# Kernel optimization log

Measured on AMD Instinct MI355X. Metric: run time of the kernel, lower is better.

The kernel has to match this reference:

```python
import jax, jax.numpy as jnp
import numpy as np
from functools import partial

V, H, B, T, L = 32000, 1024, 64, 64, 4
EOS = 2


def setup_inputs() -> dict:
    key = jax.random.key(0)
    ks = jax.random.split(key, 10)
    s = 1.0 / np.sqrt(H)
    return {
        "max_len": T,
        "tgt": jax.random.randint(ks[0], (B, T), 0, V),
        "h0": jax.random.normal(ks[1], (L, B, H), jnp.float32),
        "c0": jax.random.normal(ks[2], (L, B, H), jnp.float32),
        "embedding": jax.random.normal(ks[3], (V, H), jnp.float32) * s,
        "W_ih": jax.random.normal(ks[4], (L, 4 * H, H), jnp.float32) * s,
        "W_hh": jax.random.normal(ks[5], (L, 4 * H, H), jnp.float32) * s,
        "b_ih": jax.random.normal(ks[6], (L, 4 * H), jnp.float32) * s,
        "b_hh": jax.random.normal(ks[7], (L, 4 * H), jnp.float32) * s,
        "W_cls": jax.random.normal(ks[8], (V, H), jnp.float32) * s,
        "b_cls": jax.random.normal(ks[9], (V,), jnp.float32) * s,
    }


def _lstm_cell(x, h, c, Wi, Wh, bi, bh):
    # gates: [B, 4H] in torch order (i, f, g, o)
    g = x @ Wi.T + bi + h @ Wh.T + bh
    i, f, gg, o = jnp.split(g, 4, axis=-1)
    c2 = jax.nn.sigmoid(f) * c + jax.nn.sigmoid(i) * jnp.tanh(gg)
    h2 = jax.nn.sigmoid(o) * jnp.tanh(c2)
    return h2, c2


def reference(max_len, tgt, h0, c0, embedding, W_ih, W_hh, b_ih, b_hh, W_cls, b_cls):
    # step i>0 uses embedding of tgt[:, i-1].
    batch = tgt.shape[0]
    x0 = jnp.broadcast_to(embedding[EOS], (batch, embedding.shape[1]))
    tf_in = embedding[tgt[:, : max_len - 1]]              # [B, T-1, H]
    inputs = jnp.concatenate([x0[:, None, :], tf_in], axis=1)  # [B, T, H]
    inputs = jnp.swapaxes(inputs, 0, 1)                   # [T, B, H]

    def step(carry, x):
        h, c = carry  # each [L, B, H]
        hs, cs = [], []
        inp = x
        for l in range(L):  # 4 stacked LSTM cells, h of cell l feeds cell l+1
            hn, cn = _lstm_cell(inp, h[l], c[l], W_ih[l], W_hh[l], b_ih[l], b_hh[l])
            hs.append(hn)
            cs.append(cn)
            inp = hn
        h = jnp.stack(hs)
        c = jnp.stack(cs)
        logp = jax.nn.log_softmax(h[L - 1] @ W_cls.T + b_cls, axis=-1)  # [B, V]
        return (h, c), logp

    (h, c), out = jax.lax.scan(step, (h0, c0), inputs)
    return out, h, c  # out: [T, B, V]
```

## Files before the change

kernel.cpp:

```cpp
#include <hip/hip_runtime.h>

using u16 = unsigned short;
using u32 = unsigned int;

typedef __bf16 bf16x8 __attribute__((ext_vector_type(8)));
typedef float  f32x4  __attribute__((ext_vector_type(4)));
typedef u16    u16x8  __attribute__((ext_vector_type(8)));

static constexpr int kV = 32000, kH = 1024, kB = 64, kT = 64, kL = 4, kEOS = 2;

struct Flag { int v; int pad[15]; };

__device__ __forceinline__ u16 f2bf(float f) {
  u32 u = __float_as_uint(f);
  u = (u + 0x7fffu + ((u >> 16) & 1u)) >> 16;
  return (u16)u;
}
__device__ __forceinline__ float sigf(float x)   { return 1.0f / (1.0f + __expf(-x)); }
__device__ __forceinline__ float tanhf_(float x) { return 1.0f - 2.0f / (__expf(2.0f * x) + 1.0f); }

typedef const __attribute__((address_space(1))) u32* gas_ptr;
typedef __attribute__((address_space(3))) u32*       las_ptr;
__device__ __forceinline__ void async16(const u16* g, u16* l) {
  __builtin_amdgcn_global_load_lds((gas_ptr)g, (las_ptr)l, 16, 0, 0);
}

__device__ __forceinline__ void spin_ge(const int* p, int tgt) {
  while (__hip_atomic_load(p, __ATOMIC_RELAXED, __HIP_MEMORY_SCOPE_AGENT) < tgt)
    __builtin_amdgcn_s_sleep(2);
}

__device__ __forceinline__ size_t packed_off(int b, int k) {
  return (size_t)(((b >> 4) * 32 + (k >> 5)) * 512 + (((k >> 3) & 3) * 16 + (b & 15)) * 8 + (k & 7));
}


__global__ void pack_lstm(const float* __restrict__ Wih, const float* __restrict__ Whh,
                          u16* __restrict__ wpack) {
  const int cid  = blockIdx.x * 256 + threadIdx.x;
  const int lane = cid & 63;
  const int cf   = (cid >> 6) & 3;
  const int kk   = (cid >> 8) & 31;
  const int mt   = (cid >> 13) & 1;
  const int blk  = cid >> 14;
  const int lay = blk >> 6, cb = blk & 63;
  const int wr = cf * 1024 + cb * 16 + (lane & 15);
  const int kb = kk * 32 + (lane >> 4) * 8;
  const float* src = (mt ? Whh : Wih) + ((size_t)lay * 4096 + wr) * 1024 + kb;
  const float4* s4 = (const float4*)src;
  float4 v0 = s4[0], v1 = s4[1];
  u16x8 r;
  r[0]=f2bf(v0.x); r[1]=f2bf(v0.y); r[2]=f2bf(v0.z); r[3]=f2bf(v0.w);
  r[4]=f2bf(v1.x); r[5]=f2bf(v1.y); r[6]=f2bf(v1.z); r[7]=f2bf(v1.w);
  *(u16x8*)(wpack + (size_t)cid * 8) = r;
}

__global__ void pack_cls(const float* __restrict__ W, u16* __restrict__ o) {
  const size_t cid = (size_t)blockIdx.x * 256 + threadIdx.x;
  const float4* s4 = (const float4*)(W + cid * 8);
  float4 v0 = s4[0], v1 = s4[1];
  u16x8 r;
  r[0]=f2bf(v0.x); r[1]=f2bf(v0.y); r[2]=f2bf(v0.z); r[3]=f2bf(v0.w);
  r[4]=f2bf(v1.x); r[5]=f2bf(v1.y); r[6]=f2bf(v1.z); r[7]=f2bf(v1.w);
  *(u16x8*)(o + cid * 8) = r;
}

__global__ void pack_x(const float* __restrict__ emb, const int* __restrict__ tgt,
                       u16* __restrict__ X) {
  const int cid = blockIdx.x * 256 + threadIdx.x;
  const int kc = cid & 127, b = (cid >> 7) & 63, t = cid >> 13;
  const int tok = (t == 0) ? kEOS : tgt[b * 64 + t - 1];
  const float4* s4 = (const float4*)(emb + (size_t)tok * 1024 + kc * 8);
  float4 v0 = s4[0], v1 = s4[1];
  u16x8 r;
  r[0]=f2bf(v0.x); r[1]=f2bf(v0.y); r[2]=f2bf(v0.z); r[3]=f2bf(v0.w);
  r[4]=f2bf(v1.x); r[5]=f2bf(v1.y); r[6]=f2bf(v1.z); r[7]=f2bf(v1.w);
  *(u16x8*)(X + (size_t)t * 65536 + packed_off(b, kc * 8)) = r;
}

__global__ void pack_init(const float* __restrict__ h0, const float* __restrict__ bih,
                          const float* __restrict__ bhh, u16* __restrict__ hball,
                          float* __restrict__ bsum) {
  const int cid = blockIdx.x * 256 + threadIdx.x;
  if (cid < 32768) {
    const int kc = cid & 127, row = cid >> 7;
    const int lay = row >> 6, b = row & 63;
    const float4* s4 = (const float4*)(h0 + (size_t)cid * 8);
    float4 v0 = s4[0], v1 = s4[1];
    u16x8 r;
    r[0]=f2bf(v0.x); r[1]=f2bf(v0.y); r[2]=f2bf(v0.z); r[3]=f2bf(v0.w);
    r[4]=f2bf(v1.x); r[5]=f2bf(v1.y); r[6]=f2bf(v1.z); r[7]=f2bf(v1.w);
    *(u16x8*)(hball + (size_t)lay * 65 * 65536 + packed_off(b, kc * 8)) = r;
  } else {
    const int i = cid - 32768;
    bsum[i] = bih[i] + bhh[i];
  }
}

__global__ void __launch_bounds__(512)
lstm_coop(const u16* __restrict__ wpack, const u16* __restrict__ xall,
          u16* __restrict__ hball, const float* __restrict__ bsum,
          const float* __restrict__ c0, float* __restrict__ outh, float* __restrict__ outc,
          Flag* flags) {
  __shared__ u16 stg[3][32][512];
  __shared__ float Gc[2][64][68];

  const int tid = threadIdx.x, lane = tid & 63, wave = tid >> 6;
  const int l15 = lane & 15, l4 = lane >> 4;
  const int cmat = wave >> 2, cwc = (wave >> 1) & 1, ckh = wave & 1;
  const int blk = blockIdx.x, lay = blk >> 6, cb = blk & 63, u0 = cb << 4;
  const int ub = tid >> 3, uu = (tid & 7) * 2;

  float creg0 = c0[((size_t)lay * 64 + ub) * 1024 + u0 + uu];
  float creg1 = c0[((size_t)lay * 64 + ub) * 1024 + u0 + uu + 1];
  float bsv[8];
  #pragma unroll
  for (int g = 0; g < 4; ++g) {
    bsv[g]     = bsum[lay * 4096 + g * 1024 + u0 + uu];
    bsv[4 + g] = bsum[lay * 4096 + g * 1024 + u0 + uu + 1];
  }

  const size_t wbase = (size_t)blk * 131072;
  bf16x8 breg[2][16];
  #pragma unroll
  for (int ci = 0; ci < 2; ++ci)
    #pragma unroll
    for (int j = 0; j < 16; ++j)
      breg[ci][j] = *(const bf16x8*)(wpack + wbase
          + (size_t)(((cmat * 32 + 2 * j + ckh) * 4) + cwc * 2 + ci) * 512 + lane * 8);

  u16* hlay = hball + (size_t)lay * 65 * 65536;
  const u16* hprev = (lay == 0) ? xall : (hball + (size_t)(lay - 1) * 65 * 65536);

  #pragma unroll 1
  for (int t = 0; t < kT; ++t) {
    if (t > 0 && tid < 64)               spin_ge(&flags[lay * 64 + tid].v, t);
    if (lay > 0 && tid >= 64 && tid < 128) spin_ge(&flags[(lay - 1) * 64 + (tid - 64)].v, t + 1);
    __syncthreads();

    const u16* xsrc = (lay == 0) ? (xall + (size_t)t * 65536)
                                 : (hprev + (size_t)(t + 1) * 65536);
    const u16* hsrc = hlay + (size_t)t * 65536;

    auto STAGE = [&](int c) {
      #pragma unroll
      for (int q = 0; q < 4; ++q) {
        const int j = wave * 4 + q;
        const int m2 = j >> 4, mt = (j >> 2) & 3, ksl = j & 3;
        const u16* g = (m2 ? hsrc : xsrc) + (size_t)((mt * 32 + c * 4 + ksl) * 512) + lane * 8;
        async16(g, &stg[c % 3][m2 * 16 + mt * 4 + ksl][0]);
      }
    };

    f32x4 acc[4][2] = {};
    STAGE(0); STAGE(1);
    #pragma unroll
    for (int c = 0; c < 8; ++c) {
      if (c < 7) asm volatile("s_waitcnt vmcnt(4)" ::: "memory");
      else       asm volatile("s_waitcnt vmcnt(0)" ::: "memory");
      __builtin_amdgcn_s_barrier();
      asm volatile("" ::: "memory");
      if (c < 6) STAGE(c + 2);
      const u16* As = &stg[c % 3][cmat * 16][0];
      #pragma unroll
      for (int s = 0; s < 2; ++s) {
        const int ksl = 2 * s + ckh;
        bf16x8 a[4];
        #pragma unroll
        for (int m = 0; m < 4; ++m)
          a[m] = *(const bf16x8*)(As + (m * 4 + ksl) * 512 + lane * 8);
        #pragma unroll
        for (int m = 0; m < 4; ++m) {
          acc[m][0] = __builtin_amdgcn_mfma_f32_16x16x32_bf16(a[m], breg[0][2 * c + s], acc[m][0], 0, 0, 0);
          acc[m][1] = __builtin_amdgcn_mfma_f32_16x16x32_bf16(a[m], breg[1][2 * c + s], acc[m][1], 0, 0, 0);
        }
      }
    }

    if (ckh == 0) {
      #pragma unroll
      for (int m = 0; m < 4; ++m)
        #pragma unroll
        for (int ci = 0; ci < 2; ++ci)
          #pragma unroll
          for (int r = 0; r < 4; ++r)
            Gc[cmat][m * 16 + l4 * 4 + r][cwc * 32 + ci * 16 + l15] = acc[m][ci][r];
    }
    __syncthreads();
    if (ckh == 1) {
      #pragma unroll
      for (int m = 0; m < 4; ++m)
        #pragma unroll
        for (int ci = 0; ci < 2; ++ci)
          #pragma unroll
          for (int r = 0; r < 4; ++r)
            Gc[cmat][m * 16 + l4 * 4 + r][cwc * 32 + ci * 16 + l15] += acc[m][ci][r];
    }
    __syncthreads();

    float2 sg[4];
    #pragma unroll
    for (int g = 0; g < 4; ++g) {
      const int col = g * 16 + uu;
      const float2 v0 = *(const float2*)&Gc[0][ub][col];
      const float2 v1 = *(const float2*)&Gc[1][ub][col];
      sg[g] = make_float2(v0.x + v1.x, v0.y + v1.y);
    }
    u16 hv[2];
    #pragma unroll
    for (int p = 0; p < 2; ++p) {
      const float gi = (p ? sg[0].y : sg[0].x) + bsv[p * 4 + 0];
      const float gf = (p ? sg[1].y : sg[1].x) + bsv[p * 4 + 1];
      const float gg = (p ? sg[2].y : sg[2].x) + bsv[p * 4 + 2];
      const float go = (p ? sg[3].y : sg[3].x) + bsv[p * 4 + 3];
      const float cr = (p == 0) ? creg0 : creg1;
      const float c2 = sigf(gf) * cr + sigf(gi) * tanhf_(gg);
      const float h2 = sigf(go) * tanhf_(c2);
      if (p == 0) creg0 = c2; else creg1 = c2;
      hv[p] = f2bf(h2);
      if (t == kT - 1) {
        outh[((size_t)lay * 64 + ub) * 1024 + u0 + uu + p] = h2;
        outc[((size_t)lay * 64 + ub) * 1024 + u0 + uu + p] = c2;
      }
    }
    const u32 hpair = (u32)hv[0] | ((u32)hv[1] << 16);
    u32* hdst = (u32*)(hlay + (size_t)(t + 1) * 65536 + packed_off(ub, u0 + uu));
    __hip_atomic_store(hdst, hpair, __ATOMIC_RELAXED, __HIP_MEMORY_SCOPE_AGENT);

    __syncthreads();
    if (tid == 0)
      __hip_atomic_store(&flags[lay * 64 + cb].v, t + 1, __ATOMIC_RELAXED, __HIP_MEMORY_SCOPE_AGENT);
  }
}

__global__ void __launch_bounds__(256)
cls_gemm(const u16* __restrict__ A, const u16* __restrict__ Bw,
         const float* __restrict__ bcls, float* __restrict__ out) {
  __shared__ u16 sA[2][4096], sB[2][4096];
  const int tid = threadIdx.x, lane = tid & 63, wave = tid >> 6;
  const int wm = wave >> 1, wc = wave & 1;
  const int l15 = lane & 15, l4 = lane >> 4;
  const int bn = blockIdx.x, bm = blockIdx.y;
  const u16* Ab = A  + (size_t)bm * 131072;
  const u16* Bb = Bw + (size_t)bn * 131072;

  auto STAGE = [&](int kk) {
    u16* dA = sA[kk & 1]; u16* dB = sB[kk & 1];
    #pragma unroll
    for (int q = 0; q < 4; ++q) {
      const int u = wave * 4 + q;
      if (u < 8) {
        const u16* g = Ab + (size_t)(u >> 2) * 65536 + (size_t)(((u & 3) * 32 + kk) * 512) + lane * 8;
        async16(g, dA + u * 512);
      } else {
        const int v = u & 7;
        const u16* g = Bb + (size_t)((v & 1) * 64 + lane) * 1024 + kk * 32 + (v >> 1) * 8;
        async16(g, dB + v * 512);
      }
    }
  };

  f32x4 acc[4][4] = {};
  STAGE(0);
  for (int kk = 0; kk < 32; ++kk) {
    if (kk < 31) { STAGE(kk + 1); asm volatile("s_waitcnt vmcnt(4)" ::: "memory"); }
    else         asm volatile("s_waitcnt vmcnt(0)" ::: "memory");
    __builtin_amdgcn_s_barrier();
    asm volatile("" ::: "memory");
    const u16* aS = sA[kk & 1]; const u16* bS = sB[kk & 1];
    bf16x8 av[4], bv[4];
    #pragma unroll
    for (int mi = 0; mi < 4; ++mi) av[mi] = *(const bf16x8*)(aS + (wm * 4 + mi) * 512 + lane * 8);
    #pragma unroll
    for (int ci = 0; ci < 4; ++ci) bv[ci] = *(const bf16x8*)(bS + l4 * 1024 + (wc * 64 + ci * 16 + l15) * 8);
    #pragma unroll
    for (int mi = 0; mi < 4; ++mi)
      #pragma unroll
      for (int ci = 0; ci < 4; ++ci)
        acc[mi][ci] = __builtin_amdgcn_mfma_f32_16x16x32_bf16(av[mi], bv[ci], acc[mi][ci], 0, 0, 0);
    asm volatile("" ::: "memory");
    __builtin_amdgcn_s_barrier();
  }
  #pragma unroll
  for (int ci = 0; ci < 4; ++ci) {
    const int col = bn * 128 + wc * 64 + ci * 16 + l15;
    const float bc = bcls[col];
    #pragma unroll
    for (int mi = 0; mi < 4; ++mi) {
      #pragma unroll
      for (int r = 0; r < 4; ++r) {
        const int row = bm * 128 + wm * 64 + mi * 16 + l4 * 4 + r;
        out[(size_t)row * 32000 + col] = acc[mi][ci][r] + bc;
      }
    }
  }
}

__global__ void __launch_bounds__(256)
cls_gemm_f32(const u16* __restrict__ A, const float* __restrict__ Bw,
             const float* __restrict__ bcls, float* __restrict__ out) {
  __shared__ u16 sA[2][4096], sB[2][4096];
  const int tid = threadIdx.x, lane = tid & 63, wave = tid >> 6;
  const int wm = wave >> 1, wc = wave & 1;
  const int l15 = lane & 15, l4 = lane >> 4;
  const int bn = blockIdx.x, bm = blockIdx.y;
  const u16*  Ab = A  + (size_t)bm * 131072;
  const float* Bb = Bw + (size_t)bn * 131072;

  auto LOADB = [&](int kk, u16x8* rb) {
    #pragma unroll
    for (int q = 0; q < 2; ++q) {
      const int p = tid + q * 256, row = p & 127, khi = p >> 7;
      const float4* s4 = (const float4*)(Bb + (size_t)row * 1024 + kk * 32 + khi * 8);
      float4 v0 = s4[0], v1 = s4[1];
      u16x8 r;
      r[0]=f2bf(v0.x); r[1]=f2bf(v0.y); r[2]=f2bf(v0.z); r[3]=f2bf(v0.w);
      r[4]=f2bf(v1.x); r[5]=f2bf(v1.y); r[6]=f2bf(v1.z); r[7]=f2bf(v1.w);
      rb[q] = r;
    }
  };
  auto WRITEB = [&](int kk, const u16x8* rb) {
    u16* dB = sB[kk & 1];
    #pragma unroll
    for (int q = 0; q < 2; ++q) {
      const int p = tid + q * 256;
      *(u16x8*)(dB + p * 8) = rb[q];
    }
  };
  auto STAGE_A = [&](int kk) {
    u16* dA = sA[kk & 1];
    #pragma unroll
    for (int q = 0; q < 2; ++q) {
      const int v = wave * 2 + q;
      const u16* g = Ab + (size_t)(v >> 2) * 65536 + (size_t)(((v & 3) * 32 + kk) * 512) + lane * 8;
      async16(g, dA + v * 512);
    }
  };

  f32x4 acc[4][4] = {};
  {
    u16x8 rb[2];
    LOADB(0, rb); STAGE_A(0); WRITEB(0, rb);
  }
  for (int kk = 0; kk < 32; ++kk) {
    if (kk < 31) {
      u16x8 rb[2];
      LOADB(kk + 1, rb);
      STAGE_A(kk + 1);
      WRITEB(kk + 1, rb);
    } else {
      asm volatile("s_waitcnt vmcnt(0)" ::: "memory");
    }
    __builtin_amdgcn_s_barrier();
    asm volatile("" ::: "memory");
    const u16* aS = sA[kk & 1]; const u16* bS = sB[kk & 1];
    bf16x8 av[4], bv[4];
    #pragma unroll
    for (int mi = 0; mi < 4; ++mi) av[mi] = *(const bf16x8*)(aS + (wm * 4 + mi) * 512 + lane * 8);
    #pragma unroll
    for (int ci = 0; ci < 4; ++ci) bv[ci] = *(const bf16x8*)(bS + l4 * 1024 + (wc * 64 + ci * 16 + l15) * 8);
    #pragma unroll
    for (int mi = 0; mi < 4; ++mi)
      #pragma unroll
      for (int ci = 0; ci < 4; ++ci)
        acc[mi][ci] = __builtin_amdgcn_mfma_f32_16x16x32_bf16(av[mi], bv[ci], acc[mi][ci], 0, 0, 0);
    asm volatile("" ::: "memory");
    __builtin_amdgcn_s_barrier();
  }
  #pragma unroll
  for (int ci = 0; ci < 4; ++ci) {
    const int col = bn * 128 + wc * 64 + ci * 16 + l15;
    const float bc = bcls[col];
    #pragma unroll
    for (int mi = 0; mi < 4; ++mi) {
      #pragma unroll
      for (int r = 0; r < 4; ++r) {
        const int row = bm * 128 + wm * 64 + mi * 16 + l4 * 4 + r;
        out[(size_t)row * 32000 + col] = acc[mi][ci][r] + bc;
      }
    }
  }
}

__global__ void __launch_bounds__(256)
lsm_k(float* __restrict__ out) {
  __shared__ float red[256];
  const int r = blockIdx.x;
  float* p = out + (size_t)r * 32000;
  const float4* p4 = (const float4*)p;
  float m = -3.0e38f;
  for (int v = threadIdx.x; v < 8000; v += 256) {
    const float4 x = p4[v];
    m = fmaxf(m, fmaxf(fmaxf(x.x, x.y), fmaxf(x.z, x.w)));
  }
  red[threadIdx.x] = m; __syncthreads();
  for (int s2 = 128; s2 > 0; s2 >>= 1) {
    if ((int)threadIdx.x < s2) red[threadIdx.x] = fmaxf(red[threadIdx.x], red[threadIdx.x + s2]);
    __syncthreads();
  }
  m = red[0]; __syncthreads();
  float s = 0.0f;
  for (int v = threadIdx.x; v < 8000; v += 256) {
    const float4 x = p4[v];
    s += __expf(x.x - m) + __expf(x.y - m) + __expf(x.z - m) + __expf(x.w - m);
  }
  red[threadIdx.x] = s; __syncthreads();
  for (int s2 = 128; s2 > 0; s2 >>= 1) {
    if ((int)threadIdx.x < s2) red[threadIdx.x] += red[threadIdx.x + s2];
    __syncthreads();
  }
  const float z = m + logf(red[0]);
  float4* q4 = (float4*)p;
  for (int v = threadIdx.x; v < 8000; v += 256) {
    float4 x = p4[v];
    x.x -= z; x.y -= z; x.z -= z; x.w -= z;
    q4[v] = x;
  }
}

extern "C" void kernel_launch(void* const* d_in, const int* in_sizes, int n_in,
                              void* d_out, int out_size, void* d_ws, size_t ws_size,
                              hipStream_t stream) {
  (void)in_sizes; (void)n_in; (void)out_size;
  const int*   tgt  = (const int*)d_in[1];
  const float* h0   = (const float*)d_in[2];
  const float* c0   = (const float*)d_in[3];
  const float* emb  = (const float*)d_in[4];
  const float* Wih  = (const float*)d_in[5];
  const float* Whh  = (const float*)d_in[6];
  const float* bih  = (const float*)d_in[7];
  const float* bhh  = (const float*)d_in[8];
  const float* Wcls = (const float*)d_in[9];
  const float* bcls = (const float*)d_in[10];

  float* out  = (float*)d_out;
  float* outh = out + (size_t)kT * kB * kV;
  float* outc = outh + (size_t)kL * kB * kH;

  const size_t SZ_WPACK = 67108864;
  const size_t SZ_WCLS  = 65536000;
  const size_t SZ_X     = 8388608;
  const size_t SZ_HBALL = 34078720;
  const size_t SZ_BSUM  = 65536;
  const size_t SZ_FLAGS = 16384;
  const size_t FULL_REQ = SZ_WPACK + SZ_WCLS + SZ_X + SZ_HBALL + SZ_BSUM + SZ_FLAGS;
  const bool full = (ws_size >= FULL_REQ);

  char* ws = (char*)d_ws;
  size_t off = 0;
  u16* wpack = (u16*)(ws + off); off += SZ_WPACK;
  u16* wclsb = nullptr;
  if (full) { wclsb = (u16*)(ws + off); off += SZ_WCLS; }
  u16*   X     = (u16*)(ws + off); off += SZ_X;
  u16*   hball = (u16*)(ws + off); off += SZ_HBALL;
  float* bsum  = (float*)(ws + off); off += SZ_BSUM;
  Flag*  flags = (Flag*)(ws + off);  off += SZ_FLAGS;

  pack_lstm<<<16384, 256, 0, stream>>>(Wih, Whh, wpack);
  if (full) pack_cls<<<16000, 256, 0, stream>>>(Wcls, wclsb);
  pack_x   <<<2048,  256, 0, stream>>>(emb, tgt, X);
  pack_init<<<192,   256, 0, stream>>>(h0, bih, bhh, hball, bsum);
  hipMemsetAsync(flags, 0, SZ_FLAGS, stream);

  void* args[] = { (void*)&wpack, (void*)&X, (void*)&hball, (void*)&bsum,
                   (void*)&c0, (void*)&outh, (void*)&outc, (void*)&flags };
  hipLaunchCooperativeKernel((const void*)lstm_coop, dim3(256), dim3(512), args, 0, stream);

  const u16* h3a = hball + (size_t)3 * 65 * 65536 + 65536;
  if (full) cls_gemm    <<<dim3(250, 32), 256, 0, stream>>>(h3a, wclsb, bcls, out);
  else      cls_gemm_f32<<<dim3(250, 32), 256, 0, stream>>>(h3a, Wcls,  bcls, out);
  lsm_k<<<4096, 256, 0, stream>>>(out);
}
```

Measured before the change: 1.451 ms.

## Fuse log-softmax partial reductions into classifier GEMM and widen LSTM blocks

The classifier GEMM epilogue now computes per-tile row max and sum-exp partials. A small reduction kernel combines them into log-normalizers, and a final pass subtracts them, replacing the three-pass log-softmax that re-read the logits twice. Separately, the cooperative LSTM kernel moves to 1024 threads per block with 16 waves that each own one column tile, double- rather than triple-buffered staging, and a single four-way LDS reduction of gate partials. This cuts register pressure per wave and one barrier per step, but adds per-row syncthreads in the GEMM epilogue and a shallower load pipeline.

```diff
diff --git a/kernel.cpp b/kernel.cpp
--- a/kernel.cpp
+++ b/kernel.cpp
@@ -97,44 +97,42 @@
   }
 }
 
-__global__ void __launch_bounds__(512)
+__global__ void __launch_bounds__(1024, 4)
 lstm_coop(const u16* __restrict__ wpack, const u16* __restrict__ xall,
           u16* __restrict__ hball, const float* __restrict__ bsum,
           const float* __restrict__ c0, float* __restrict__ outh, float* __restrict__ outc,
           Flag* flags) {
-  __shared__ u16 stg[3][32][512];
-  __shared__ float Gc[2][64][68];
+  __shared__ u16 stg[2][32][512];
+  __shared__ float Gc[4][64][66];
 
   const int tid = threadIdx.x, lane = tid & 63, wave = tid >> 6;
   const int l15 = lane & 15, l4 = lane >> 4;
-  const int cmat = wave >> 2, cwc = (wave >> 1) & 1, ckh = wave & 1;
+  const int cmat = wave >> 3, cwc = (wave >> 1) & 3, ckh = wave & 1;
   const int blk = blockIdx.x, lay = blk >> 6, cb = blk & 63, u0 = cb << 4;
-  const int ub = tid >> 3, uu = (tid & 7) * 2;
-
-  float creg0 = c0[((size_t)lay * 64 + ub) * 1024 + u0 + uu];
-  float creg1 = c0[((size_t)lay * 64 + ub) * 1024 + u0 + uu + 1];
-  float bsv[8];
-  #pragma unroll
-  for (int g = 0; g < 4; ++g) {
-    bsv[g]     = bsum[lay * 4096 + g * 1024 + u0 + uu];
-    bsv[4 + g] = bsum[lay * 4096 + g * 1024 + u0 + uu + 1];
-  }
+  const int ub = tid >> 4, uu = tid & 15;
+
+  float creg = c0[((size_t)lay * 64 + ub) * 1024 + u0 + uu];
+  float bsv[4];
+  #pragma unroll
+  for (int g = 0; g < 4; ++g) bsv[g] = bsum[lay * 4096 + g * 1024 + u0 + uu];
 
   const size_t wbase = (size_t)blk * 131072;
-  bf16x8 breg[2][16];
-  #pragma unroll
-  for (int ci = 0; ci < 2; ++ci)
-    #pragma unroll
-    for (int j = 0; j < 16; ++j)
-      breg[ci][j] = *(const bf16x8*)(wpack + wbase
-          + (size_t)(((cmat * 32 + 2 * j + ckh) * 4) + cwc * 2 + ci) * 512 + lane * 8);
+  bf16x8 breg[16];
+  #pragma unroll
+  for (int j = 0; j < 16; ++j)
+    breg[j] = *(const bf16x8*)(wpack + wbase
+        + (size_t)(((cmat * 32 + 2 * j + ckh) * 4) + cwc) * 512 + lane * 8);
+
+  const int j0 = wave * 2, j1 = wave * 2 + 1;
+  const int m2a = j0 >> 4, mta = (j0 >> 2) & 3, ksla = j0 & 3;
+  const int m2b = j1 >> 4, mtb = (j1 >> 2) & 3, kslb = j1 & 3;
 
   u16* hlay = hball + (size_t)lay * 65 * 65536;
   const u16* hprev = (lay == 0) ? xall : (hball + (size_t)(lay - 1) * 65 * 65536);
 
   #pragma unroll 1
   for (int t = 0; t < kT; ++t) {
-    if (t > 0 && tid < 64)               spin_ge(&flags[lay * 64 + tid].v, t);
+    if (t > 0 && tid < 64)                 spin_ge(&flags[lay * 64 + tid].v, t);
     if (lay > 0 && tid >= 64 && tid < 128) spin_ge(&flags[(lay - 1) * 64 + (tid - 64)].v, t + 1);
     __syncthreads();
 
@@ -142,26 +140,25 @@
                                  : (hprev + (size_t)(t + 1) * 65536);
     const u16* hsrc = hlay + (size_t)t * 65536;
 
+    const u16* ga = (m2a ? hsrc : xsrc) + (size_t)((mta * 32 + ksla) * 512) + lane * 8;
+    const u16* gb = (m2b ? hsrc : xsrc) + (size_t)((mtb * 32 + kslb) * 512) + lane * 8;
+    u16* da = &stg[0][m2a * 16 + mta * 4 + ksla][0];
+    u16* db = &stg[0][m2b * 16 + mtb * 4 + kslb][0];
+
     auto STAGE = [&](int c) {
-      #pragma unroll
-      for (int q = 0; q < 4; ++q) {
-        const int j = wave * 4 + q;
-        const int m2 = j >> 4, mt = (j >> 2) & 3, ksl = j & 3;
-        const u16* g = (m2 ? hsrc : xsrc) + (size_t)((mt * 32 + c * 4 + ksl) * 512) + lane * 8;
-        async16(g, &stg[c % 3][m2 * 16 + mt * 4 + ksl][0]);
-      }
+      async16(ga + (size_t)c * 2048, da + (c & 1) * 16384);
+      async16(gb + (size_t)c * 2048, db + (c & 1) * 16384);
     };
 
-    f32x4 acc[4][2] = {};
-    STAGE(0); STAGE(1);
+    f32x4 acc[4] = {};
+    STAGE(0);
     #pragma unroll
     for (int c = 0; c < 8; ++c) {
-      if (c < 7) asm volatile("s_waitcnt vmcnt(4)" ::: "memory");
-      else       asm volatile("s_waitcnt vmcnt(0)" ::: "memory");
+      asm volatile("s_waitcnt vmcnt(0)" ::: "memory");
       __builtin_amdgcn_s_barrier();
       asm volatile("" ::: "memory");
-      if (c < 6) STAGE(c + 2);
-      const u16* As = &stg[c % 3][cmat * 16][0];
+      if (c < 7) STAGE(c + 1);
+      const u16* As = &stg[c & 1][cmat * 16][0];
       #pragma unroll
       for (int s = 0; s < 2; ++s) {
         const int ksl = 2 * s + ckh;
@@ -170,72 +167,83 @@
         for (int m = 0; m < 4; ++m)
           a[m] = *(const bf16x8*)(As + (m * 4 + ksl) * 512 + lane * 8);
         #pragma unroll
-        for (int m = 0; m < 4; ++m) {
-          acc[m][0] = __builtin_amdgcn_mfma_f32_16x16x32_bf16(a[m], breg[0][2 * c + s], acc[m][0], 0, 0, 0);
-          acc[m][1] = __builtin_amdgcn_mfma_f32_16x16x32_bf16(a[m], breg[1][2 * c + s], acc[m][1], 0, 0, 0);
-        }
+        for (int m = 0; m < 4; ++m)
+          acc[m] = __builtin_amdgcn_mfma_f32_16x16x32_bf16(a[m], breg[2 * c + s], acc[m], 0, 0, 0);
       }
     }
 
-    if (ckh == 0) {
+    {
+      const int q = cmat * 2 + ckh;
       #pragma unroll
       for (int m = 0; m < 4; ++m)
         #pragma unroll
-        for (int ci = 0; ci < 2; ++ci)
-          #pragma unroll
-          for (int r = 0; r < 4; ++r)
-            Gc[cmat][m * 16 + l4 * 4 + r][cwc * 32 + ci * 16 + l15] = acc[m][ci][r];
+        for (int r = 0; r < 4; ++r)
+          Gc[q][m * 16 + l4 * 4 + r][cwc * 16 + l15] = acc[m][r];
     }
     __syncthreads();
-    if (ckh == 1) {
-      #pragma unroll
-      for (int m = 0; m < 4; ++m)
-        #pragma unroll
-        for (int ci = 0; ci < 2; ++ci)
-          #pragma unroll
-          for (int r = 0; r < 4; ++r)
-            Gc[cmat][m * 16 + l4 * 4 + r][cwc * 32 + ci * 16 + l15] += acc[m][ci][r];
-    }
-    __syncthreads();
-
-    float2 sg[4];
+
+    float sg[4];
     #pragma unroll
     for (int g = 0; g < 4; ++g) {
       const int col = g * 16 + uu;
-      const float2 v0 = *(const float2*)&Gc[0][ub][col];
-      const float2 v1 = *(const float2*)&Gc[1][ub][col];
-      sg[g] = make_float2(v0.x + v1.x, v0.y + v1.y);
-    }
-    u16 hv[2];
-    #pragma unroll
-    for (int p = 0; p < 2; ++p) {
-      const float gi = (p ? sg[0].y : sg[0].x) + bsv[p * 4 + 0];
-      const float gf = (p ? sg[1].y : sg[1].x) + bsv[p * 4 + 1];
-      const float gg = (p ? sg[2].y : sg[2].x) + bsv[p * 4 + 2];
-      const float go = (p ? sg[3].y : sg[3].x) + bsv[p * 4 + 3];
-      const float cr = (p == 0) ? creg0 : creg1;
-      const float c2 = sigf(gf) * cr + sigf(gi) * tanhf_(gg);
-      const float h2 = sigf(go) * tanhf_(c2);
-      if (p == 0) creg0 = c2; else creg1 = c2;
-      hv[p] = f2bf(h2);
-      if (t == kT - 1) {
-        outh[((size_t)lay * 64 + ub) * 1024 + u0 + uu + p] = h2;
-        outc[((size_t)lay * 64 + ub) * 1024 + u0 + uu + p] = c2;
-      }
-    }
-    const u32 hpair = (u32)hv[0] | ((u32)hv[1] << 16);
-    u32* hdst = (u32*)(hlay + (size_t)(t + 1) * 65536 + packed_off(ub, u0 + uu));
-    __hip_atomic_store(hdst, hpair, __ATOMIC_RELAXED, __HIP_MEMORY_SCOPE_AGENT);
-
+      sg[g] = Gc[0][ub][col] + Gc[1][ub][col] + Gc[2][ub][col] + Gc[3][ub][col] + bsv[g];
+    }
+    const float c2 = sigf(sg[1]) * creg + sigf(sg[0]) * tanhf_(sg[2]);
+    const float h2 = sigf(sg[3]) * tanhf_(c2);
+    creg = c2;
+    const u16 hv = f2bf(h2);
+    if (t == kT - 1) {
+      outh[((size_t)lay * 64 + ub) * 1024 + u0 + uu] = h2;
+      outc[((size_t)lay * 64 + ub) * 1024 + u0 + uu] = c2;
+    }
+    const u32 other = __shfl_xor((u32)hv, 1);
+    if ((tid & 1) == 0) {
+      const u32 hpair = (u32)hv | (other << 16);
+      u32* hdst = (u32*)(hlay + (size_t)(t + 1) * 65536 + packed_off(ub, u0 + uu));
+      __hip_atomic_store(hdst, hpair, __ATOMIC_RELAXED, __HIP_MEMORY_SCOPE_AGENT);
+    }
     __syncthreads();
     if (tid == 0)
       __hip_atomic_store(&flags[lay * 64 + cb].v, t + 1, __ATOMIC_RELAXED, __HIP_MEMORY_SCOPE_AGENT);
   }
 }
 
+#define CLS_EPILOGUE()                                                                     \
+  {                                                                                        \
+    float* sR = (float*)&sA[0][0];                                                         \
+    _Pragma("unroll")                                                                      \
+    for (int mi = 0; mi < 4; ++mi) {                                                       \
+      _Pragma("unroll")                                                                    \
+      for (int r = 0; r < 4; ++r) {                                                        \
+        float v[4];                                                                        \
+        _Pragma("unroll")                                                                  \
+        for (int ci = 0; ci < 4; ++ci) v[ci] = acc[mi][ci][r] + bc[ci];                     \
+        float mx = fmaxf(fmaxf(v[0], v[1]), fmaxf(v[2], v[3]));                            \
+        mx = fmaxf(mx, __shfl_xor(mx, 1)); mx = fmaxf(mx, __shfl_xor(mx, 2));              \
+        mx = fmaxf(mx, __shfl_xor(mx, 4)); mx = fmaxf(mx, __shfl_xor(mx, 8));              \
+        float ss = __expf(v[0]-mx) + __expf(v[1]-mx) + __expf(v[2]-mx) + __expf(v[3]-mx);  \
+        ss += __shfl_xor(ss, 1); ss += __shfl_xor(ss, 2);                                  \
+        ss += __shfl_xor(ss, 4); ss += __shfl_xor(ss, 8);                                  \
+        const int lr = wm * 64 + mi * 16 + l4 * 4 + r;                                     \
+        if (wc == 0 && l15 == 0) { sR[lr * 2] = mx; sR[lr * 2 + 1] = ss; }                 \
+        __syncthreads();                                                                   \
+        if (wc == 1 && l15 == 0) {                                                         \
+          const float m0 = sR[lr * 2], s0 = sR[lr * 2 + 1];                                \
+          const float M = fmaxf(m0, mx);                                                   \
+          const float S = s0 * __expf(m0 - M) + ss * __expf(mx - M);                       \
+          const int grow = bm * 128 + lr;                                                  \
+          pmax[(size_t)grow * 256 + bn] = M;                                               \
+          psum[(size_t)grow * 256 + bn] = S;                                               \
+        }                                                                                  \
+        __syncthreads();                                                                   \
+      }                                                                                    \
+    }                                                                                      \
+  }
+
 __global__ void __launch_bounds__(256)
 cls_gemm(const u16* __restrict__ A, const u16* __restrict__ Bw,
-         const float* __restrict__ bcls, float* __restrict__ out) {
+         const float* __restrict__ bcls, float* __restrict__ out,
+         float* __restrict__ pmax, float* __restrict__ psum) {
   __shared__ u16 sA[2][4096], sB[2][4096];
   const int tid = threadIdx.x, lane = tid & 63, wave = tid >> 6;
   const int wm = wave >> 1, wc = wave & 1;
@@ -281,24 +289,28 @@
     asm volatile("" ::: "memory");
     __builtin_amdgcn_s_barrier();
   }
+  float bc[4];
+  #pragma unroll
+  for (int ci = 0; ci < 4; ++ci) bc[ci] = bcls[bn * 128 + wc * 64 + ci * 16 + l15];
   #pragma unroll
   for (int ci = 0; ci < 4; ++ci) {
     const int col = bn * 128 + wc * 64 + ci * 16 + l15;
-    const float bc = bcls[col];
-    #pragma unroll
-    for (int mi = 0; mi < 4; ++mi) {
+    #pragma unroll
+    for (int mi = 0; mi < 4; ++mi)
       #pragma unroll
       for (int r = 0; r < 4; ++r) {
         const int row = bm * 128 + wm * 64 + mi * 16 + l4 * 4 + r;
-        out[(size_t)row * 32000 + col] = acc[mi][ci][r] + bc;
+        out[(size_t)row * 32000 + col] = acc[mi][ci][r] + bc[ci];
       }
-    }
-  }
+  }
+  __syncthreads();
+  CLS_EPILOGUE()
 }
 
 __global__ void __launch_bounds__(256)
 cls_gemm_f32(const u16* __restrict__ A, const float* __restrict__ Bw,
-             const float* __restrict__ bcls, float* __restrict__ out) {
+             const float* __restrict__ bcls, float* __restrict__ out,
+             float* __restrict__ pmax, float* __restrict__ psum) {
   __shared__ u16 sA[2][4096], sB[2][4096];
   const int tid = threadIdx.x, lane = tid & 63, wave = tid >> 6;
   const int wm = wave >> 1, wc = wave & 1;
@@ -322,10 +334,7 @@
   auto WRITEB = [&](int kk, const u16x8* rb) {
     u16* dB = sB[kk & 1];
     #pragma unroll
-    for (int q = 0; q < 2; ++q) {
-      const int p = tid + q * 256;
-      *(u16x8*)(dB + p * 8) = rb[q];
-    }
+    for (int q = 0; q < 2; ++q) *(u16x8*)(dB + (tid + q * 256) * 8) = rb[q];
   };
   auto STAGE_A = [&](int kk) {
     u16* dA = sA[kk & 1];
@@ -367,54 +376,53 @@
     asm volatile("" ::: "memory");
     __builtin_amdgcn_s_barrier();
   }
+  float bc[4];
+  #pragma unroll
+  for (int ci = 0; ci < 4; ++ci) bc[ci] = bcls[bn * 128 + wc * 64 + ci * 16 + l15];
   #pragma unroll
   for (int ci = 0; ci < 4; ++ci) {
     const int col = bn * 128 + wc * 64 + ci * 16 + l15;
-    const float bc = bcls[col];
-    #pragma unroll
-    for (int mi = 0; mi < 4; ++mi) {
+    #pragma unroll
+    for (int mi = 0; mi < 4; ++mi)
       #pragma unroll
       for (int r = 0; r < 4; ++r) {
         const int row = bm * 128 + wm * 64 + mi * 16 + l4 * 4 + r;
-        out[(size_t)row * 32000 + col] = acc[mi][ci][r] + bc;
+        out[(size_t)row * 32000 + col] = acc[mi][ci][r] + bc[ci];
       }
-    }
-  }
+  }
+  __syncthreads();
+  CLS_EPILOGUE()
 }
 
 __global__ void __launch_bounds__(256)
-lsm_k(float* __restrict__ out) {
-  __shared__ float red[256];
+lsm_red(const float* __restrict__ pmax, const float* __restrict__ psum,
+        float* __restrict__ logz) {
+  __shared__ float rm[256], rs[256];
+  const int r = blockIdx.x, b = threadIdx.x;
+  float m = -3.0e38f, s = 0.0f;
+  if (b < 250) { m = pmax[(size_t)r * 256 + b]; s = psum[(size_t)r * 256 + b]; }
+  rm[b] = m; rs[b] = s; __syncthreads();
+  for (int st = 128; st > 0; st >>= 1) {
+    if (b < st) {
+      const float m2 = rm[b + st], s2 = rs[b + st];
+      const float M = fmaxf(rm[b], m2);
+      rs[b] = rs[b] * __expf(rm[b] - M) + s2 * __expf(m2 - M);
+      rm[b] = M;
+    }
+    __syncthreads();
+  }
+  if (b == 0) logz[r] = rm[0] + logf(rs[0]);
+}
+
+__global__ void __launch_bounds__(256)
+sub_k(float* __restrict__ out, const float* __restrict__ logz) {
   const int r = blockIdx.x;
-  float* p = out + (size_t)r * 32000;
-  const float4* p4 = (const float4*)p;
-  float m = -3.0e38f;
+  const float z = logz[r];
+  float4* p = (float4*)(out + (size_t)r * 32000);
   for (int v = threadIdx.x; v < 8000; v += 256) {
-    const float4 x = p4[v];
-    m = fmaxf(m, fmaxf(fmaxf(x.x, x.y), fmaxf(x.z, x.w)));
-  }
-  red[threadIdx.x] = m; __syncthreads();
-  for (int s2 = 128; s2 > 0; s2 >>= 1) {
-    if ((int)threadIdx.x < s2) red[threadIdx.x] = fmaxf(red[threadIdx.x], red[threadIdx.x + s2]);
-    __syncthreads();
-  }
-  m = red[0]; __syncthreads();
-  float s = 0.0f;
-  for (int v = threadIdx.x; v < 8000; v += 256) {
-    const float4 x = p4[v];
-    s += __expf(x.x - m) + __expf(x.y - m) + __expf(x.z - m) + __expf(x.w - m);
-  }
-  red[threadIdx.x] = s; __syncthreads();
-  for (int s2 = 128; s2 > 0; s2 >>= 1) {
-    if ((int)threadIdx.x < s2) red[threadIdx.x] += red[threadIdx.x + s2];
-    __syncthreads();
-  }
-  const float z = m + logf(red[0]);
-  float4* q4 = (float4*)p;
-  for (int v = threadIdx.x; v < 8000; v += 256) {
-    float4 x = p4[v];
+    float4 x = p[v];
     x.x -= z; x.y -= z; x.z -= z; x.w -= z;
-    q4[v] = x;
+    p[v] = x;
   }
 }
 
@@ -443,7 +451,8 @@
   const size_t SZ_HBALL = 34078720;
   const size_t SZ_BSUM  = 65536;
   const size_t SZ_FLAGS = 16384;
-  const size_t FULL_REQ = SZ_WPACK + SZ_WCLS + SZ_X + SZ_HBALL + SZ_BSUM + SZ_FLAGS;
+  const size_t SZ_PM    = 4194304;
+  const size_t FULL_REQ = SZ_WPACK + SZ_WCLS + SZ_X + SZ_HBALL + SZ_BSUM + SZ_FLAGS + 2 * SZ_PM + 16384;
   const bool full = (ws_size >= FULL_REQ);
 
   char* ws = (char*)d_ws;
@@ -455,6 +464,9 @@
   u16*   hball = (u16*)(ws + off); off += SZ_HBALL;
   float* bsum  = (float*)(ws + off); off += SZ_BSUM;
   Flag*  flags = (Flag*)(ws + off);  off += SZ_FLAGS;
+  float* pmax  = (float*)(ws + off); off += SZ_PM;
+  float* psum  = (float*)(ws + off); off += SZ_PM;
+  float* logz  = (float*)(ws + off); off += 16384;
 
   pack_lstm<<<16384, 256, 0, stream>>>(Wih, Whh, wpack);
   if (full) pack_cls<<<16000, 256, 0, stream>>>(Wcls, wclsb);
@@ -464,10 +476,11 @@
 
   void* args[] = { (void*)&wpack, (void*)&X, (void*)&hball, (void*)&bsum,
                    (void*)&c0, (void*)&outh, (void*)&outc, (void*)&flags };
-  hipLaunchCooperativeKernel((const void*)lstm_coop, dim3(256), dim3(512), args, 0, stream);
+  hipLaunchCooperativeKernel((const void*)lstm_coop, dim3(256), dim3(1024), args, 0, stream);
 
   const u16* h3a = hball + (size_t)3 * 65 * 65536 + 65536;
-  if (full) cls_gemm    <<<dim3(250, 32), 256, 0, stream>>>(h3a, wclsb, bcls, out);
-  else      cls_gemm_f32<<<dim3(250, 32), 256, 0, stream>>>(h3a, Wcls,  bcls, out);
-  lsm_k<<<4096, 256, 0, stream>>>(out);
-}
+  if (full) cls_gemm    <<<dim3(250, 32), 256, 0, stream>>>(h3a, wclsb, bcls, out, pmax, psum);
+  else      cls_gemm_f32<<<dim3(250, 32), 256, 0, stream>>>(h3a, Wcls,  bcls, out, pmax, psum);
+  lsm_red<<<4096, 256, 0, stream>>>(pmax, psum, logz);
+  sub_k  <<<4096, 256, 0, stream>>>(out, logz);
+}
```

Measured after the change: 1.414 ms. 2.5% less time.
